# Kernel tuning notes

Hardware: AMD Instinct MI355X
Metric: run time of the kernel (lower is better)

Reference implementation:

```python
import jax, jax.numpy as jnp
import numpy as np

B, SQ, SK, D, H, F = 8, 512, 1024, 1024, 16, 4096
DK = D // H
NEG_INF = -jnp.inf


def _linear(x, w, b):
    return x @ w + b


def _mha(q, k, v, wq, bq, wk, bk, wv, bv, wo, bo, causal, kv_mask):
    # q: [B,Sq,D], k/v: [B,Sk,D]
    b, sq, d = q.shape
    sk = k.shape[1]
    Q = _linear(q, wq, bq).reshape(b, sq, H, DK).transpose(0, 2, 1, 3)  # [B,H,Sq,dk]
    K = _linear(k, wk, bk).reshape(b, sk, H, DK).transpose(0, 2, 1, 3)
    V = _linear(v, wv, bv).reshape(b, sk, H, DK).transpose(0, 2, 1, 3)
    S = jnp.einsum('bhqd,bhkd->bhqk', Q, K) / jnp.sqrt(jnp.asarray(DK, Q.dtype))
    if kv_mask is not None:
        S = jnp.where(kv_mask[:, None, None, :] == 0, NEG_INF, S)
    if causal:
        tri = jnp.tril(jnp.ones((sq, sk), dtype=bool))
        S = jnp.where(tri, S, NEG_INF)
    A = jax.nn.softmax(S, axis=-1)  # dropout p=0 -> identity
    x = jnp.einsum('bhqk,bhkd->bhqd', A, V).transpose(0, 2, 1, 3).reshape(b, sq, d)
    return _linear(x, wo, bo), A


def _ln(x, g, beta, eps=1e-5):
    mu = jnp.mean(x, axis=-1, keepdims=True)
    var = jnp.mean(jnp.square(x - mu), axis=-1, keepdims=True)
    return (x - mu) * jax.lax.rsqrt(var + eps) * g + beta


def setup_inputs() -> dict:
    key = jax.random.key(0)
    ks = jax.random.split(key, 32)
    s = 0.02
    inp = {
        'x': jax.random.normal(ks[0], (B, SQ, D), jnp.float32),
        'enc_o': jax.random.normal(ks[1], (B, SK, D), jnp.float32),
        'enc_mask': jax.random.randint(ks[2], (B, SK), 0, 2, jnp.int32),
    }
    i = 3
    for pfx in ('a1', 'a2'):
        for nm in ('wq', 'wk', 'wv', 'wo'):
            inp[f'{pfx}_{nm}'] = jax.random.normal(ks[i], (D, D), jnp.float32) * s; i += 1
            inp[f'{pfx}_{nm[1:] and "b" + nm[1:]}'] = jnp.zeros((D,), jnp.float32)
    inp['ff_w1'] = jax.random.normal(ks[i], (D, F), jnp.float32) * s; i += 1
    inp['ff_b1'] = jnp.zeros((F,), jnp.float32)
    inp['ff_w2'] = jax.random.normal(ks[i], (F, D), jnp.float32) * s; i += 1
    inp['ff_b2'] = jnp.zeros((D,), jnp.float32)
    for n in ('ln1', 'ln2', 'ln3'):
        inp[f'{n}_g'] = jnp.ones((D,), jnp.float32)
        inp[f'{n}_b'] = jnp.zeros((D,), jnp.float32)
    return inp


def reference(x, enc_o, enc_mask,
              a1_wq, a1_bq, a1_wk, a1_bk, a1_wv, a1_bv, a1_wo, a1_bo,
              a2_wq, a2_bq, a2_wk, a2_bk, a2_wv, a2_bv, a2_wo, a2_bo,
              ff_w1, ff_b1, ff_w2, ff_b2,
              ln1_g, ln1_b, ln2_g, ln2_b, ln3_g, ln3_b):
    res, _ = _mha(x, x, x, a1_wq, a1_bq, a1_wk, a1_bk, a1_wv, a1_bv, a1_wo, a1_bo,
                  causal=True, kv_mask=None)
    x = _ln(x + res, ln1_g, ln1_b)
    res, attn = _mha(x, enc_o, enc_o, a2_wq, a2_bq, a2_wk, a2_bk, a2_wv, a2_bv, a2_wo, a2_bo,
                     causal=False, kv_mask=enc_mask)
    x = _ln(x + res, ln2_g, ln2_b)
    res = _linear(jax.nn.relu(_linear(x, ff_w1, ff_b1)), ff_w2, ff_b2)
    x = _ln(x + res, ln3_g, ln3_b)
    return (x, attn)
```

## Files before the change

kernel.cpp:

```cpp
#include <hip/hip_runtime.h>
#include <hip/hip_bf16.h>


using bf16 = __hip_bfloat16;
typedef __attribute__((ext_vector_type(8))) short short8;
typedef __attribute__((ext_vector_type(4))) float f32x4;

#define DEVINL __device__ __forceinline__

DEVINL unsigned short bf16bits(float f) {
  __hip_bfloat16 h = __float2bfloat16(f);
  return *reinterpret_cast<unsigned short*>(&h);
}
DEVINL float bits2f(unsigned short u) {
  return __uint_as_float(((unsigned int)u) << 16);
}
DEVINL float tofloat(float f) { return f; }
DEVINL float tofloat(bf16 h) { return __bfloat162float(h); }

#define GLD16(gp, lp) __builtin_amdgcn_global_load_lds( \
    (__attribute__((address_space(1))) const void*)(gp), \
    (__attribute__((address_space(3))) void*)(lp), 16, 0, 0)

struct GemmP {
  const bf16* A; const bf16* Bt; void* C;
  const float* bias; const int* kmask;
  float scale;
  int M, N, K, lda, ldb, ldc;
  long sAb, sAh, sBb, sBh, sCb, sCh;
};

enum { EPI_BIAS_BF16 = 0, EPI_CAUSAL_BF16, EPI_KMASK_F32, EPI_NONE_BF16,
       EPI_BIAS_F32, EPI_BIAS_RELU_BF16, EPI_PART_F32 };

template<int EPI>
__global__ __launch_bounds__(256)
void gemm_k(GemmP p) {
  __shared__ bf16 As[128 * 32];
  __shared__ bf16 Bs[128 * 32];
  const int t = threadIdx.x;
  const int lane = t & 63;
  const int w = t >> 6;
  const int z = blockIdx.z;
  const int zb = z >> 4, zh = z & 15;
  const int m0 = blockIdx.y * 128, n0 = blockIdx.x * 128;

  const bf16* Ab = p.A + (long)zb * p.sAb + (long)zh * p.sAh;
  const bf16* Bb = p.Bt + (long)zb * p.sBb + (long)zh * p.sBh;
  const int fl = lane & 15, fq = lane >> 4;
  const int wm = (w >> 1) * 64, wn = (w & 1) * 64;

  f32x4 acc[4][4];
#pragma unroll
  for (int i = 0; i < 4; ++i)
#pragma unroll
    for (int j = 0; j < 4; ++j) acc[i][j] = (f32x4){0.f, 0.f, 0.f, 0.f};

  const int sr = t >> 2;
  const int sc = (t & 3) * 8;
  char* ldsA = (char*)As + w * 1024;
  char* ldsB = (char*)Bs + w * 1024;

  int brow0 = n0 + sr;      if (brow0 > p.N - 1) brow0 = p.N - 1;
  int brow1 = n0 + sr + 64; if (brow1 > p.N - 1) brow1 = p.N - 1;

  for (int k0 = 0; k0 < p.K; k0 += 32) {
    GLD16(Ab + (long)(m0 + sr) * p.lda + k0 + sc, ldsA);
    GLD16(Ab + (long)(m0 + sr + 64) * p.lda + k0 + sc, ldsA + 4096);
    GLD16(Bb + (long)brow0 * p.ldb + k0 + sc, ldsB);
    GLD16(Bb + (long)brow1 * p.ldb + k0 + sc, ldsB + 4096);
    __syncthreads();

    short8 af[4], bfv[4];
#pragma unroll
    for (int i = 0; i < 4; ++i)
      af[i] = *(const short8*)(As + (wm + i * 16 + fl) * 32 + fq * 8);
#pragma unroll
    for (int j = 0; j < 4; ++j)
      bfv[j] = *(const short8*)(Bs + (wn + j * 16 + fl) * 32 + fq * 8);
#pragma unroll
    for (int i = 0; i < 4; ++i)
#pragma unroll
      for (int j = 0; j < 4; ++j)
        acc[i][j] = __builtin_amdgcn_mfma_f32_16x16x32_bf16(af[i], bfv[j], acc[i][j], 0, 0, 0);
    __syncthreads();
  }

  const float NEGINF = -__builtin_inff();
  const long cbase = (long)zb * p.sCb + (long)zh * p.sCh;
#pragma unroll
  for (int i = 0; i < 4; ++i) {
#pragma unroll
    for (int j = 0; j < 4; ++j) {
#pragma unroll
      for (int r = 0; r < 4; ++r) {
        int row = m0 + wm + i * 16 + fq * 4 + r;
        int col = n0 + wn + j * 16 + fl;
        if (col < p.N) {
          float v = acc[i][j][r];
          if (EPI == EPI_BIAS_BF16 || EPI == EPI_BIAS_F32 || EPI == EPI_BIAS_RELU_BF16)
            v += p.bias[col];
          if (EPI == EPI_BIAS_RELU_BF16) v = v > 0.f ? v : 0.f;
          if (EPI == EPI_CAUSAL_BF16) { v *= p.scale; if (col > row) v = NEGINF; }
          if (EPI == EPI_KMASK_F32)   { v *= p.scale; if (p.kmask[zb * 1024 + col] == 0) v = NEGINF; }
          long off = cbase + (long)row * p.ldc + col;
          if (EPI == EPI_KMASK_F32 || EPI == EPI_BIAS_F32 || EPI == EPI_PART_F32)
            ((float*)p.C)[off] = v;
          else ((bf16*)p.C)[off] = __float2bfloat16(v);
        }
      }
    }
  }
}

__global__ __launch_bounds__(256) void softmax_self_k(bf16* A) {
  const int lane = threadIdx.x & 63;
  const long row = (long)blockIdx.x * 4 + (threadIdx.x >> 6);
  bf16* p = A + row * 512;
  short8 raw = *(const short8*)(p + lane * 8);
  float v[8];
#pragma unroll
  for (int i = 0; i < 8; ++i) v[i] = bits2f((unsigned short)raw[i]);
  float mx = v[0];
#pragma unroll
  for (int i = 1; i < 8; ++i) mx = fmaxf(mx, v[i]);
  for (int off = 32; off; off >>= 1) mx = fmaxf(mx, __shfl_xor(mx, off, 64));
  float s = 0.f;
#pragma unroll
  for (int i = 0; i < 8; ++i) { v[i] = expf(v[i] - mx); s += v[i]; }
  for (int off = 32; off; off >>= 1) s += __shfl_xor(s, off, 64);
  float inv = 1.f / s;
  short8 o;
#pragma unroll
  for (int i = 0; i < 8; ++i) o[i] = (short)bf16bits(v[i] * inv);
  *(short8*)(p + lane * 8) = o;
}

__global__ __launch_bounds__(256) void softmax_cross_k(float* A, bf16* Pb) {
  const int lane = threadIdx.x & 63;
  const long row = (long)blockIdx.x * 4 + (threadIdx.x >> 6);
  float* p = A + row * 1024;
  float4 v[4];
#pragma unroll
  for (int c = 0; c < 4; ++c) v[c] = *(const float4*)(p + c * 256 + lane * 4);
  float mx = v[0].x;
#pragma unroll
  for (int c = 0; c < 4; ++c) {
    mx = fmaxf(mx, v[c].x); mx = fmaxf(mx, v[c].y);
    mx = fmaxf(mx, v[c].z); mx = fmaxf(mx, v[c].w);
  }
  for (int off = 32; off; off >>= 1) mx = fmaxf(mx, __shfl_xor(mx, off, 64));
  float s = 0.f;
#pragma unroll
  for (int c = 0; c < 4; ++c) {
    v[c].x = expf(v[c].x - mx); s += v[c].x;
    v[c].y = expf(v[c].y - mx); s += v[c].y;
    v[c].z = expf(v[c].z - mx); s += v[c].z;
    v[c].w = expf(v[c].w - mx); s += v[c].w;
  }
  for (int off = 32; off; off >>= 1) s += __shfl_xor(s, off, 64);
  float inv = 1.f / s;
#pragma unroll
  for (int c = 0; c < 4; ++c) {
    v[c].x *= inv; v[c].y *= inv; v[c].z *= inv; v[c].w *= inv;
    *(float4*)(p + c * 256 + lane * 4) = v[c];
    uint2 pk;
    pk.x = bf16bits(v[c].x) | ((unsigned)bf16bits(v[c].y) << 16);
    pk.y = bf16bits(v[c].z) | ((unsigned)bf16bits(v[c].w) << 16);
    *(uint2*)(Pb + row * 1024 + c * 256 + lane * 4) = pk;
  }
}

__global__ __launch_bounds__(256)
void ln_k(const float* __restrict__ x, const float* __restrict__ r,
          const float* __restrict__ g, const float* __restrict__ bt,
          float* __restrict__ outf, bf16* __restrict__ outb) {
  const int lane = threadIdx.x & 63;
  const long row = (long)blockIdx.x * 4 + (threadIdx.x >> 6);
  const float* px = x + row * 1024;
  const float* pr = r + row * 1024;
  float4 v[4];
  float s = 0.f;
#pragma unroll
  for (int c = 0; c < 4; ++c) {
    float4 a = *(const float4*)(px + c * 256 + lane * 4);
    float4 b = *(const float4*)(pr + c * 256 + lane * 4);
    v[c].x = a.x + b.x; v[c].y = a.y + b.y; v[c].z = a.z + b.z; v[c].w = a.w + b.w;
    s += v[c].x + v[c].y + v[c].z + v[c].w;
  }
  for (int off = 32; off; off >>= 1) s += __shfl_xor(s, off, 64);
  float mu = s * (1.f / 1024.f);
  float q = 0.f;
#pragma unroll
  for (int c = 0; c < 4; ++c) {
    float dx = v[c].x - mu, dy = v[c].y - mu, dz = v[c].z - mu, dw = v[c].w - mu;
    q += dx * dx + dy * dy + dz * dz + dw * dw;
  }
  for (int off = 32; off; off >>= 1) q += __shfl_xor(q, off, 64);
  float rs = rsqrtf(q * (1.f / 1024.f) + 1e-5f);
#pragma unroll
  for (int c = 0; c < 4; ++c) {
    int col = c * 256 + lane * 4;
    float4 gg = *(const float4*)(g + col);
    float4 bb = *(const float4*)(bt + col);
    float4 o;
    o.x = (v[c].x - mu) * rs * gg.x + bb.x;
    o.y = (v[c].y - mu) * rs * gg.y + bb.y;
    o.z = (v[c].z - mu) * rs * gg.z + bb.z;
    o.w = (v[c].w - mu) * rs * gg.w + bb.w;
    *(float4*)(outf + row * 1024 + col) = o;
    if (outb) {
      uint2 pk;
      pk.x = bf16bits(o.x) | ((unsigned)bf16bits(o.y) << 16);
      pk.y = bf16bits(o.z) | ((unsigned)bf16bits(o.w) << 16);
      *(uint2*)(outb + row * 1024 + col) = pk;
    }
  }
}

template<typename TI>
__global__ __launch_bounds__(256)
void transpose_k(const TI* __restrict__ in, bf16* __restrict__ out,
                 int R, int C, int ldi, int ldo,
                 long sInb, long sInh, long sOutb, long sOuth) {
  __shared__ float tile[32][33];
  const int zb = blockIdx.z >> 4, zh = blockIdx.z & 15;
  const TI* pin = in + (long)zb * sInb + (long)zh * sInh;
  bf16* pout = out + (long)zb * sOutb + (long)zh * sOuth;
  const int c0 = blockIdx.x * 32, r0 = blockIdx.y * 32;
  const int tx = threadIdx.x & 31, ty = threadIdx.x >> 5;
#pragma unroll
  for (int i = 0; i < 32; i += 8)
    tile[ty + i][tx] = tofloat(pin[(long)(r0 + ty + i) * ldi + c0 + tx]);
  __syncthreads();
#pragma unroll
  for (int i = 0; i < 32; i += 8)
    pout[(long)(c0 + ty + i) * ldo + r0 + tx] = __float2bfloat16(tile[tx][ty + i]);
}

__global__ __launch_bounds__(256) void cvt_k(const float* __restrict__ in,
                                             bf16* __restrict__ out, long n4) {
  long i = (long)blockIdx.x * 256 + threadIdx.x;
  if (i < n4) {
    float4 v = *(const float4*)(in + i * 4);
    uint2 pk;
    pk.x = bf16bits(v.x) | ((unsigned)bf16bits(v.y) << 16);
    pk.y = bf16bits(v.z) | ((unsigned)bf16bits(v.w) << 16);
    *(uint2*)(out + i * 4) = pk;
  }
}

__global__ __launch_bounds__(256)
void concatb_k(float* dst, const float* a, const float* b, const float* c,
               int n, int total) {
  int i = blockIdx.x * 256 + threadIdx.x;
  if (i >= total) return;
  float v = (i < n) ? a[i] : (i < 2 * n ? b[i - n] : c[i - 2 * n]);
  dst[i] = v;
}

__global__ __launch_bounds__(256)
void reduce4_k(const float* __restrict__ part, const float* __restrict__ bias,
               float* __restrict__ out) {
  long i = ((long)blockIdx.x * 256 + threadIdx.x) * 4;
  float4 a = *(const float4*)(part + i);
  float4 b = *(const float4*)(part + 4194304 + i);
  float4 c = *(const float4*)(part + 2 * 4194304 + i);
  float4 d = *(const float4*)(part + 3 * 4194304 + i);
  float4 bi = *(const float4*)(bias + (int)(i & 1023));
  float4 o;
  o.x = a.x + b.x + c.x + d.x + bi.x;
  o.y = a.y + b.y + c.y + d.y + bi.y;
  o.z = a.z + b.z + c.z + d.z + bi.z;
  o.w = a.w + b.w + c.w + d.w + bi.w;
  *(float4*)(out + i) = o;
}

static inline GemmP mkp(const void* A, const bf16* Bt, void* C,
                        const float* bias, const int* km, float sc,
                        int M, int N, int K, int lda, int ldb, int ldc,
                        long sAb, long sAh, long sBb, long sBh, long sCb, long sCh) {
  GemmP p;
  p.A = (const bf16*)A; p.Bt = Bt; p.C = C; p.bias = bias; p.kmask = km; p.scale = sc;
  p.M = M; p.N = N; p.K = K; p.lda = lda; p.ldb = ldb; p.ldc = ldc;
  p.sAb = sAb; p.sAh = sAh; p.sBb = sBb; p.sBh = sBh; p.sCb = sCb; p.sCh = sCh;
  return p;
}

extern "C" void kernel_launch(void* const* d_in, const int* in_sizes, int n_in,
                              void* d_out, int out_size, void* d_ws, size_t ws_size,
                              hipStream_t stream) {
  const float* x        = (const float*)d_in[0];
  const float* enc_o    = (const float*)d_in[1];
  const int*   enc_mask = (const int*)d_in[2];
  const float* a1_wq = (const float*)d_in[3];  const float* a1_bq = (const float*)d_in[4];
  const float* a1_wk = (const float*)d_in[5];  const float* a1_bk = (const float*)d_in[6];
  const float* a1_wv = (const float*)d_in[7];  const float* a1_bv = (const float*)d_in[8];
  const float* a1_wo = (const float*)d_in[9];  const float* a1_bo = (const float*)d_in[10];
  const float* a2_wq = (const float*)d_in[11]; const float* a2_bq = (const float*)d_in[12];
  const float* a2_wk = (const float*)d_in[13]; const float* a2_bk = (const float*)d_in[14];
  const float* a2_wv = (const float*)d_in[15]; const float* a2_bv = (const float*)d_in[16];
  const float* a2_wo = (const float*)d_in[17]; const float* a2_bo = (const float*)d_in[18];
  const float* ff_w1 = (const float*)d_in[19]; const float* ff_b1 = (const float*)d_in[20];
  const float* ff_w2 = (const float*)d_in[21]; const float* ff_b2 = (const float*)d_in[22];
  const float* ln1_g = (const float*)d_in[23]; const float* ln1_b = (const float*)d_in[24];
  const float* ln2_g = (const float*)d_in[25]; const float* ln2_b = (const float*)d_in[26];
  const float* ln3_g = (const float*)d_in[27]; const float* ln3_b = (const float*)d_in[28];

  const size_t MB = 1u << 20;
  const long M1 = 1048576;
  char* w = (char*)d_ws;
  bf16*  xb   = (bf16*)(w + 0);
  bf16*  encb = (bf16*)(w + 8 * MB);
  float* x1f  = (float*)(w + 24 * MB);
  float* x2f  = (float*)(w + 40 * MB);
  bf16*  xcb  = (bf16*)(w + 56 * MB);
  bf16*  wT   = (bf16*)(w + 64 * MB);
  float* bqkv = (float*)(w + 96 * MB);
  float* bkv  = (float*)(w + 96 * MB + 16384);
  bf16*  QKV  = (bf16*)(w + 104 * MB);
  bf16*  KVc  = (bf16*)(w + 128 * MB);
  bf16*  Vt   = (bf16*)(w + 160 * MB);
  bf16*  Ob   = (bf16*)(w + 176 * MB);
  float* res  = (float*)(w + 184 * MB);
  float* part = (float*)(w + 200 * MB);
  bf16*  Asf  = (bf16*)(w + 264 * MB);
  bf16*  Pb   = (bf16*)(w + 332 * MB);

  float* out_x = (float*)d_out;
  float* attn  = (float*)d_out + 4194304;

  const dim3 blk(256);

  cvt_k<<<4096, blk, 0, stream>>>(x, xb, 1048576);
  cvt_k<<<8192, blk, 0, stream>>>(enc_o, encb, 2097152);
  {
    dim3 tg(32, 32, 1);
    transpose_k<float><<<tg, blk, 0, stream>>>(a1_wq, wT + 0 * M1, 1024, 1024, 1024, 1024, 0,0,0,0);
    transpose_k<float><<<tg, blk, 0, stream>>>(a1_wk, wT + 1 * M1, 1024, 1024, 1024, 1024, 0,0,0,0);
    transpose_k<float><<<tg, blk, 0, stream>>>(a1_wv, wT + 2 * M1, 1024, 1024, 1024, 1024, 0,0,0,0);
    transpose_k<float><<<tg, blk, 0, stream>>>(a1_wo, wT + 3 * M1, 1024, 1024, 1024, 1024, 0,0,0,0);
    transpose_k<float><<<tg, blk, 0, stream>>>(a2_wq, wT + 4 * M1, 1024, 1024, 1024, 1024, 0,0,0,0);
    transpose_k<float><<<tg, blk, 0, stream>>>(a2_wk, wT + 5 * M1, 1024, 1024, 1024, 1024, 0,0,0,0);
    transpose_k<float><<<tg, blk, 0, stream>>>(a2_wv, wT + 6 * M1, 1024, 1024, 1024, 1024, 0,0,0,0);
    transpose_k<float><<<tg, blk, 0, stream>>>(a2_wo, wT + 7 * M1, 1024, 1024, 1024, 1024, 0,0,0,0);
    transpose_k<float><<<dim3(128, 32, 1), blk, 0, stream>>>(ff_w1, wT + 8 * M1, 1024, 4096, 4096, 1024, 0,0,0,0);
    transpose_k<float><<<dim3(32, 128, 1), blk, 0, stream>>>(ff_w2, wT + 12 * M1, 4096, 1024, 1024, 4096, 0,0,0,0);
  }
  concatb_k<<<12, blk, 0, stream>>>(bqkv, a1_bq, a1_bk, a1_bv, 1024, 3072);
  concatb_k<<<8, blk, 0, stream>>>(bkv, a2_bk, a2_bv, a2_bv, 1024, 2048);

  gemm_k<EPI_BIAS_BF16><<<dim3(24, 32, 1), blk, 0, stream>>>(
      mkp(xb, wT, QKV, bqkv, nullptr, 0.f, 4096, 3072, 1024, 1024, 1024, 3072, 0,0,0,0,0,0));
  bf16* Qs = QKV;
  bf16* Ks = QKV + 1024;
  bf16* Vs = QKV + 2048;

  gemm_k<EPI_CAUSAL_BF16><<<dim3(4, 4, 128), blk, 0, stream>>>(
      mkp(Qs, Ks, Asf, nullptr, nullptr, 0.125f, 512, 512, 64, 3072, 3072, 512,
          1572864, 64, 1572864, 64, 4194304, 262144));
  softmax_self_k<<<16384, blk, 0, stream>>>(Asf);

  transpose_k<bf16><<<dim3(2, 16, 128), blk, 0, stream>>>(
      Vs, Vt, 512, 64, 3072, 512, 1572864, 64, 524288, 32768);

  gemm_k<EPI_NONE_BF16><<<dim3(1, 4, 128), blk, 0, stream>>>(
      mkp(Asf, Vt, Ob, nullptr, nullptr, 0.f, 512, 64, 512, 512, 512, 1024,
          4194304, 262144, 524288, 32768, 524288, 64));

  gemm_k<EPI_BIAS_F32><<<dim3(8, 32, 1), blk, 0, stream>>>(
      mkp(Ob, wT + 3 * M1, res, a1_bo, nullptr, 0.f, 4096, 1024, 1024, 1024, 1024, 1024, 0,0,0,0,0,0));

  ln_k<<<1024, blk, 0, stream>>>(x, res, ln1_g, ln1_b, x1f, xcb);

  gemm_k<EPI_BIAS_BF16><<<dim3(8, 32, 1), blk, 0, stream>>>(
      mkp(xcb, wT + 4 * M1, QKV, a2_bq, nullptr, 0.f, 4096, 1024, 1024, 1024, 1024, 1024, 0,0,0,0,0,0));
  gemm_k<EPI_BIAS_BF16><<<dim3(16, 64, 1), blk, 0, stream>>>(
      mkp(encb, wT + 5 * M1, KVc, bkv, nullptr, 0.f, 8192, 2048, 1024, 1024, 1024, 2048, 0,0,0,0,0,0));
  bf16* Qc = QKV;
  bf16* Kc = KVc;
  bf16* Vc = KVc + 1024;

  gemm_k<EPI_KMASK_F32><<<dim3(8, 4, 128), blk, 0, stream>>>(
      mkp(Qc, Kc, attn, nullptr, enc_mask, 0.125f, 512, 1024, 64, 1024, 2048, 1024,
          524288, 64, 2097152, 64, 8388608, 524288));
  softmax_cross_k<<<16384, blk, 0, stream>>>(attn, Pb);

  transpose_k<bf16><<<dim3(2, 32, 128), blk, 0, stream>>>(
      Vc, Vt, 1024, 64, 2048, 1024, 2097152, 64, 1048576, 65536);

  gemm_k<EPI_NONE_BF16><<<dim3(1, 4, 128), blk, 0, stream>>>(
      mkp(Pb, Vt, Ob, nullptr, nullptr, 0.f, 512, 64, 1024, 1024, 1024, 1024,
          8388608, 524288, 1048576, 65536, 524288, 64));

  gemm_k<EPI_BIAS_F32><<<dim3(8, 32, 1), blk, 0, stream>>>(
      mkp(Ob, wT + 7 * M1, res, a2_bo, nullptr, 0.f, 4096, 1024, 1024, 1024, 1024, 1024, 0,0,0,0,0,0));

  ln_k<<<1024, blk, 0, stream>>>(x1f, res, ln2_g, ln2_b, x2f, xcb);

  gemm_k<EPI_BIAS_RELU_BF16><<<dim3(32, 32, 1), blk, 0, stream>>>(
      mkp(xcb, wT + 8 * M1, Asf, ff_b1, nullptr, 0.f, 4096, 4096, 1024, 1024, 1024, 4096, 0,0,0,0,0,0));
  gemm_k<EPI_PART_F32><<<dim3(8, 32, 4), blk, 0, stream>>>(
      mkp(Asf, wT + 12 * M1, part, nullptr, nullptr, 0.f, 4096, 1024, 1024, 4096, 4096, 1024,
          0, 1024, 0, 1024, 0, 4194304));
  reduce4_k<<<4096, blk, 0, stream>>>(part, ff_b2, res);

  ln_k<<<1024, blk, 0, stream>>>(x2f, res, ln3_g, ln3_b, out_x, nullptr);
}
```

Before: 1.153 ms.

## Fuse QK^T, softmax and PV into one attention kernel per head tile

Replaces the separate score GEMM, softmax and PV GEMM launches for both self and cross attention with a single kernel. Each block holds a 32-row score tile in LDS and streams K and V tiles through a triple-buffered ring using direct-to-LDS loads. The causal path only visits the key tiles it needs, and the bf16 score and probability intermediates no longer round-trip through global memory. The tradeoff is a large LDS footprint (128KB of scores for cross attention), which limits occupancy, and the PV step only uses 64-wide MFMA work per block.

New measurement: 1.216 ms. 5.5% more time.

```diff
diff --git a/kernel.cpp b/kernel.cpp
--- a/kernel.cpp
+++ b/kernel.cpp
@@ -11,9 +11,6 @@
 DEVINL unsigned short bf16bits(float f) {
   __hip_bfloat16 h = __float2bfloat16(f);
   return *reinterpret_cast<unsigned short*>(&h);
-}
-DEVINL float bits2f(unsigned short u) {
-  return __uint_as_float(((unsigned int)u) << 16);
 }
 DEVINL float tofloat(float f) { return f; }
 DEVINL float tofloat(bf16 h) { return __bfloat162float(h); }
@@ -113,62 +110,191 @@
   }
 }
 
-__global__ __launch_bounds__(256) void softmax_self_k(bf16* A) {
-  const int lane = threadIdx.x & 63;
-  const long row = (long)blockIdx.x * 4 + (threadIdx.x >> 6);
-  bf16* p = A + row * 512;
-  short8 raw = *(const short8*)(p + lane * 8);
-  float v[8];
-#pragma unroll
-  for (int i = 0; i < 8; ++i) v[i] = bits2f((unsigned short)raw[i]);
-  float mx = v[0];
-#pragma unroll
-  for (int i = 1; i < 8; ++i) mx = fmaxf(mx, v[i]);
-  for (int off = 32; off; off >>= 1) mx = fmaxf(mx, __shfl_xor(mx, off, 64));
-  float s = 0.f;
-#pragma unroll
-  for (int i = 0; i < 8; ++i) { v[i] = expf(v[i] - mx); s += v[i]; }
-  for (int off = 32; off; off >>= 1) s += __shfl_xor(s, off, 64);
-  float inv = 1.f / s;
-  short8 o;
-#pragma unroll
-  for (int i = 0; i < 8; ++i) o[i] = (short)bf16bits(v[i] * inv);
-  *(short8*)(p + lane * 8) = o;
-}
-
-__global__ __launch_bounds__(256) void softmax_cross_k(float* A, bf16* Pb) {
-  const int lane = threadIdx.x & 63;
-  const long row = (long)blockIdx.x * 4 + (threadIdx.x >> 6);
-  float* p = A + row * 1024;
-  float4 v[4];
-#pragma unroll
-  for (int c = 0; c < 4; ++c) v[c] = *(const float4*)(p + c * 256 + lane * 4);
-  float mx = v[0].x;
-#pragma unroll
-  for (int c = 0; c < 4; ++c) {
-    mx = fmaxf(mx, v[c].x); mx = fmaxf(mx, v[c].y);
-    mx = fmaxf(mx, v[c].z); mx = fmaxf(mx, v[c].w);
-  }
-  for (int off = 32; off; off >>= 1) mx = fmaxf(mx, __shfl_xor(mx, off, 64));
-  float s = 0.f;
-#pragma unroll
-  for (int c = 0; c < 4; ++c) {
-    v[c].x = expf(v[c].x - mx); s += v[c].x;
-    v[c].y = expf(v[c].y - mx); s += v[c].y;
-    v[c].z = expf(v[c].z - mx); s += v[c].z;
-    v[c].w = expf(v[c].w - mx); s += v[c].w;
-  }
-  for (int off = 32; off; off >>= 1) s += __shfl_xor(s, off, 64);
-  float inv = 1.f / s;
-#pragma unroll
-  for (int c = 0; c < 4; ++c) {
-    v[c].x *= inv; v[c].y *= inv; v[c].z *= inv; v[c].w *= inv;
-    *(float4*)(p + c * 256 + lane * 4) = v[c];
-    uint2 pk;
-    pk.x = bf16bits(v[c].x) | ((unsigned)bf16bits(v[c].y) << 16);
-    pk.y = bf16bits(v[c].z) | ((unsigned)bf16bits(v[c].w) << 16);
-    *(uint2*)(Pb + row * 1024 + c * 256 + lane * 4) = pk;
-  }
+struct AttnP {
+  const bf16 *Q, *K, *Vt;
+  float* Pout; bf16* O;
+  const int* kmask;
+  int ldq, ldk, ldv;
+  long sQb, sQh, sKb, sKh, sVb, sVh, sPb, sPh, sOb, sOh;
+};
+
+template<int SK, bool CAUSAL, bool WRITE_P>
+__global__ __launch_bounds__(256)
+void attn_fused_k(AttnP p) {
+  constexpr int TKMAX = SK / 64;
+  __shared__ float S[32 * SK];
+  __shared__ bf16 ring[3 * 4096];
+  const int t = threadIdx.x;
+  const int lane = t & 63;
+  const int w = t >> 6;
+  const int fl = lane & 15, fq = lane >> 4;
+  const int zb = blockIdx.z >> 4, zh = blockIdx.z & 15;
+  const int q0 = blockIdx.y * 32;
+  const float NEGINF = -__builtin_inff();
+
+  const bf16* Qb = p.Q + (long)zb * p.sQb + (long)zh * p.sQh;
+  const bf16* Kb = p.K + (long)zb * p.sKb + (long)zh * p.sKh;
+  const bf16* Vb = p.Vt + (long)zb * p.sVb + (long)zh * p.sVh;
+
+  const int Tk = CAUSAL ? ((q0 + 31) >> 6) + 1 : TKMAX;
+
+  short8 af[2][2];
+#pragma unroll
+  for (int i = 0; i < 2; ++i)
+#pragma unroll
+    for (int kk = 0; kk < 2; ++kk)
+      af[i][kk] = *(const short8*)(Qb + (long)(q0 + i * 16 + fl) * p.ldq + kk * 32 + fq * 8);
+
+  int kmv[CAUSAL ? 1 : TKMAX];
+  if (!CAUSAL) {
+#pragma unroll
+    for (int kt = 0; kt < TKMAX; ++kt)
+      kmv[kt] = p.kmask[zb * 1024 + kt * 64 + w * 16 + fl];
+  }
+
+  auto stage = [&](const bf16* mb, int ld, int roff, int coff, int buf) {
+#pragma unroll
+    for (int h = 0; h < 2; ++h) {
+      int o = h * 4096 + w * 1024 + lane * 16;
+      int r = o >> 7;
+      int cb = (o & 127) ^ ((r & 7) << 4);
+      GLD16(mb + (long)(roff + r) * ld + coff + (cb >> 1),
+            (char*)ring + buf * 8192 + h * 4096 + w * 1024);
+    }
+  };
+
+  stage(Kb, p.ldk, 0, 0, 0);
+  if (Tk > 1) stage(Kb, p.ldk, 64, 0, 1);
+  for (int kt = 0; kt < Tk; ++kt) {
+    if (kt + 1 < Tk) asm volatile("s_waitcnt vmcnt(2)" ::: "memory");
+    else             asm volatile("s_waitcnt vmcnt(0)" ::: "memory");
+    __builtin_amdgcn_s_barrier();
+    if (kt + 2 < Tk) stage(Kb, p.ldk, (kt + 2) * 64, 0, (kt + 2) % 3);
+
+    const char* kb = (const char*)ring + (kt % 3) * 8192;
+    const int krow = w * 16 + fl;
+    short8 bfv[2];
+#pragma unroll
+    for (int kk = 0; kk < 2; ++kk) {
+      int b = (krow * 128 + kk * 64 + fq * 16) ^ ((krow & 7) << 4);
+      bfv[kk] = *(const short8*)(kb + b);
+    }
+    f32x4 acc[2] = {(f32x4){0.f,0.f,0.f,0.f}, (f32x4){0.f,0.f,0.f,0.f}};
+#pragma unroll
+    for (int kk = 0; kk < 2; ++kk) {
+      acc[0] = __builtin_amdgcn_mfma_f32_16x16x32_bf16(af[0][kk], bfv[kk], acc[0], 0, 0, 0);
+      acc[1] = __builtin_amdgcn_mfma_f32_16x16x32_bf16(af[1][kk], bfv[kk], acc[1], 0, 0, 0);
+    }
+    const int col = kt * 64 + w * 16 + fl;
+    const bool mok = CAUSAL ? true : (kmv[CAUSAL ? 0 : kt] != 0);
+#pragma unroll
+    for (int i = 0; i < 2; ++i) {
+#pragma unroll
+      for (int r = 0; r < 4; ++r) {
+        int row = i * 16 + fq * 4 + r;
+        float v = acc[i][r] * 0.125f;
+        if (CAUSAL) { if (col > q0 + row) v = NEGINF; }
+        else if (!mok) v = NEGINF;
+        int e = (row * SK + col) ^ ((row & 7) << 2);
+        S[e] = v;
+      }
+    }
+  }
+
+  asm volatile("s_waitcnt lgkmcnt(0)" ::: "memory");
+  __builtin_amdgcn_s_barrier();
+
+  const int Tv = Tk;
+  stage(Vb, p.ldv, 0, 0, 0);
+  if (Tv > 1) stage(Vb, p.ldv, 0, 64, 1);
+
+  float* Prow_base = WRITE_P ? (p.Pout + (long)zb * p.sPb + (long)zh * p.sPh) : nullptr;
+  for (int rr = 0; rr < 8; ++rr) {
+    int row = w * 8 + rr;
+    int rg = q0 + row;
+    f32x4 vv[SK / 256];
+#pragma unroll
+    for (int c = 0; c < SK / 256; ++c) {
+      int col = c * 256 + lane * 4;
+      int e = (row * SK + col) ^ ((row & 7) << 2);
+      vv[c] = *(const f32x4*)&S[e];
+      if (CAUSAL) {
+#pragma unroll
+        for (int j = 0; j < 4; ++j) if (col + j > rg) vv[c][j] = NEGINF;
+      }
+    }
+    float mx = vv[0][0];
+#pragma unroll
+    for (int c = 0; c < SK / 256; ++c)
+#pragma unroll
+      for (int j = 0; j < 4; ++j) mx = fmaxf(mx, vv[c][j]);
+    for (int off = 32; off; off >>= 1) mx = fmaxf(mx, __shfl_xor(mx, off, 64));
+    float s = 0.f;
+#pragma unroll
+    for (int c = 0; c < SK / 256; ++c)
+#pragma unroll
+      for (int j = 0; j < 4; ++j) { vv[c][j] = expf(vv[c][j] - mx); s += vv[c][j]; }
+    for (int off = 32; off; off >>= 1) s += __shfl_xor(s, off, 64);
+    float inv = 1.f / s;
+#pragma unroll
+    for (int c = 0; c < SK / 256; ++c) {
+      int col = c * 256 + lane * 4;
+      int e = (row * SK + col) ^ ((row & 7) << 2);
+      f32x4 o;
+#pragma unroll
+      for (int j = 0; j < 4; ++j) o[j] = vv[c][j] * inv;
+      *(f32x4*)&S[e] = o;
+      if (WRITE_P) *(f32x4*)(Prow_base + (long)rg * SK + col) = o;
+    }
+  }
+
+  asm volatile("s_waitcnt lgkmcnt(0)" ::: "memory");
+  __builtin_amdgcn_s_barrier();
+
+  f32x4 ao[2] = {(f32x4){0.f,0.f,0.f,0.f}, (f32x4){0.f,0.f,0.f,0.f}};
+  for (int vt = 0; vt < Tv; ++vt) {
+    if (vt + 1 < Tv) asm volatile("s_waitcnt vmcnt(2)" ::: "memory");
+    else             asm volatile("s_waitcnt vmcnt(0)" ::: "memory");
+    __builtin_amdgcn_s_barrier();
+    if (vt + 2 < Tv) stage(Vb, p.ldv, 0, (vt + 2) * 64, (vt + 2) % 3);
+
+    const char* vbuf = (const char*)ring + (vt % 3) * 8192;
+    const int vrow = w * 16 + fl;
+    short8 bv[2];
+#pragma unroll
+    for (int kk = 0; kk < 2; ++kk) {
+      int b = (vrow * 128 + kk * 64 + fq * 16) ^ ((vrow & 7) << 4);
+      bv[kk] = *(const short8*)(vbuf + b);
+    }
+#pragma unroll
+    for (int i = 0; i < 2; ++i) {
+      const int row = i * 16 + fl;
+#pragma unroll
+      for (int kk = 0; kk < 2; ++kk) {
+        int c0 = vt * 64 + kk * 32 + fq * 8;
+        int e0 = (row * SK + c0) ^ ((row & 7) << 2);
+        int e1 = (row * SK + c0 + 4) ^ ((row & 7) << 2);
+        const f32x4 p0 = *(const f32x4*)&S[e0];
+        const f32x4 p1 = *(const f32x4*)&S[e1];
+        short8 pa;
+#pragma unroll
+        for (int j = 0; j < 4; ++j) {
+          pa[j]     = (short)bf16bits(p0[j]);
+          pa[4 + j] = (short)bf16bits(p1[j]);
+        }
+        ao[i] = __builtin_amdgcn_mfma_f32_16x16x32_bf16(pa, bv[kk], ao[i], 0, 0, 0);
+      }
+    }
+  }
+
+  bf16* Ob_ = p.O + (long)zb * p.sOb + (long)zh * p.sOh;
+#pragma unroll
+  for (int i = 0; i < 2; ++i)
+#pragma unroll
+    for (int r = 0; r < 4; ++r) {
+      int row = q0 + i * 16 + fq * 4 + r;
+      Ob_[(long)row * 1024 + w * 16 + fl] = __float2bfloat16(ao[i][r]);
+    }
 }
 
 __global__ __launch_bounds__(256)
@@ -325,7 +451,6 @@
   float* res  = (float*)(w + 184 * MB);
   float* part = (float*)(w + 200 * MB);
   bf16*  Asf  = (bf16*)(w + 264 * MB);
-  bf16*  Pb   = (bf16*)(w + 332 * MB);
 
   float* out_x = (float*)d_out;
   float* attn  = (float*)d_out + 4194304;
@@ -356,17 +481,18 @@
   bf16* Ks = QKV + 1024;
   bf16* Vs = QKV + 2048;
 
-  gemm_k<EPI_CAUSAL_BF16><<<dim3(4, 4, 128), blk, 0, stream>>>(
-      mkp(Qs, Ks, Asf, nullptr, nullptr, 0.125f, 512, 512, 64, 3072, 3072, 512,
-          1572864, 64, 1572864, 64, 4194304, 262144));
-  softmax_self_k<<<16384, blk, 0, stream>>>(Asf);
-
   transpose_k<bf16><<<dim3(2, 16, 128), blk, 0, stream>>>(
       Vs, Vt, 512, 64, 3072, 512, 1572864, 64, 524288, 32768);
 
-  gemm_k<EPI_NONE_BF16><<<dim3(1, 4, 128), blk, 0, stream>>>(
-      mkp(Asf, Vt, Ob, nullptr, nullptr, 0.f, 512, 64, 512, 512, 512, 1024,
-          4194304, 262144, 524288, 32768, 524288, 64));
+  {
+    AttnP ap;
+    ap.Q = Qs; ap.K = Ks; ap.Vt = Vt; ap.Pout = nullptr; ap.O = Ob; ap.kmask = nullptr;
+    ap.ldq = 3072; ap.ldk = 3072; ap.ldv = 512;
+    ap.sQb = 1572864; ap.sQh = 64; ap.sKb = 1572864; ap.sKh = 64;
+    ap.sVb = 524288;  ap.sVh = 32768; ap.sPb = 0; ap.sPh = 0;
+    ap.sOb = 524288;  ap.sOh = 64;
+    attn_fused_k<512, true, false><<<dim3(1, 16, 128), blk, 0, stream>>>(ap);
+  }
 
   gemm_k<EPI_BIAS_F32><<<dim3(8, 32, 1), blk, 0, stream>>>(
       mkp(Ob, wT + 3 * M1, res, a1_bo, nullptr, 0.f, 4096, 1024, 1024, 1024, 1024, 1024, 0,0,0,0,0,0));
@@ -381,17 +507,18 @@
   bf16* Kc = KVc;
   bf16* Vc = KVc + 1024;
 
-  gemm_k<EPI_KMASK_F32><<<dim3(8, 4, 128), blk, 0, stream>>>(
-      mkp(Qc, Kc, attn, nullptr, enc_mask, 0.125f, 512, 1024, 64, 1024, 2048, 1024,
-          524288, 64, 2097152, 64, 8388608, 524288));
-  softmax_cross_k<<<16384, blk, 0, stream>>>(attn, Pb);
-
   transpose_k<bf16><<<dim3(2, 32, 128), blk, 0, stream>>>(
       Vc, Vt, 1024, 64, 2048, 1024, 2097152, 64, 1048576, 65536);
 
-  gemm_k<EPI_NONE_BF16><<<dim3(1, 4, 128), blk, 0, stream>>>(
-      mkp(Pb, Vt, Ob, nullptr, nullptr, 0.f, 512, 64, 1024, 1024, 1024, 1024,
-          8388608, 524288, 1048576, 65536, 524288, 64));
+  {
+    AttnP ap;
+    ap.Q = Qc; ap.K = Kc; ap.Vt = Vt; ap.Pout = attn; ap.O = Ob; ap.kmask = enc_mask;
+    ap.ldq = 1024; ap.ldk = 2048; ap.ldv = 1024;
+    ap.sQb = 524288;  ap.sQh = 64; ap.sKb = 2097152; ap.sKh = 64;
+    ap.sVb = 1048576; ap.sVh = 65536; ap.sPb = 8388608; ap.sPh = 524288;
+    ap.sOb = 524288;  ap.sOh = 64;
+    attn_fused_k<1024, false, true><<<dim3(1, 16, 128), blk, 0, stream>>>(ap);
+  }
 
   gemm_k<EPI_BIAS_F32><<<dim3(8, 32, 1), blk, 0, stream>>>(
       mkp(Ob, wT + 7 * M1, res, a2_bo, nullptr, 0.f, 4096, 1024, 1024, 1024, 1024, 1024, 0,0,0,0,0,0));
```
